# Optimization experiments

Measured on AMD Instinct MI355X. Metric: run time of the kernel, lower is better.

The kernel has to match this reference:

```python
import jax, jax.numpy as jnp
import numpy as np

DIM = 1024
HEADS = 16
DIM_HEAD = 64
INNER = HEADS * DIM_HEAD  # 1024
EPS = 1e-5


def layer_norm(x, gamma, beta):
    mu = jnp.mean(x, axis=-1, keepdims=True)
    var = jnp.mean(jnp.square(x - mu), axis=-1, keepdims=True)
    return (x - mu) * jax.lax.rsqrt(var + EPS) * gamma + beta


def setup_inputs() -> dict:
    key = jax.random.key(0)
    ks = jax.random.split(key, 6)
    b, n1, n2 = 8, 4096, 256
    x = jax.random.normal(ks[0], (b, n1, DIM), dtype=jnp.float32)
    latents = jax.random.normal(ks[1], (b, n2, DIM), dtype=jnp.float32)
    s = 1.0 / np.sqrt(DIM)
    Wq = jax.random.normal(ks[2], (DIM, INNER), dtype=jnp.float32) * s
    Wkv = jax.random.normal(ks[3], (DIM, 2 * INNER), dtype=jnp.float32) * s
    Wout = jax.random.normal(ks[4], (INNER, DIM), dtype=jnp.float32) * (1.0 / np.sqrt(INNER))
    g1 = jnp.ones((DIM,), jnp.float32); b1 = jnp.zeros((DIM,), jnp.float32)
    g2 = jnp.ones((DIM,), jnp.float32); b2 = jnp.zeros((DIM,), jnp.float32)
    return {"x": x, "latents": latents, "g1": g1, "b1": b1, "g2": g2, "b2": b2,
            "Wq": Wq, "Wkv": Wkv, "Wout": Wout}


def reference(x, latents, g1, b1, g2, b2, Wq, Wkv, Wout):
    b, l, _ = latents.shape
    xn = layer_norm(x, g1, b1)
    ln = layer_norm(latents, g2, b2)
    q = ln @ Wq  # (b, n2, inner)
    kv_input = jnp.concatenate([xn, ln], axis=1)  # (b, n1+n2, D)
    kv = kv_input @ Wkv
    k, v = jnp.split(kv, 2, axis=-1)
    # split heads -> (b, h, len, dh)
    def heads(t):
        return t.reshape(t.shape[0], t.shape[1], HEADS, DIM_HEAD).transpose(0, 2, 1, 3)
    q, k, v = heads(q), heads(k), heads(v)
    scale = 1.0 / np.sqrt(np.sqrt(DIM_HEAD))
    logits = jnp.einsum('bhqd,bhkd->bhqk', q * scale, k * scale)
    w = jax.nn.softmax(logits.astype(jnp.float32), axis=-1).astype(logits.dtype)
    out = jnp.einsum('bhqk,bhkd->bhqd', w, v)
    out = out.transpose(0, 2, 1, 3).reshape(b, l, INNER)
    return out @ Wout
```

## Files before the change

kernel.cpp:

```cpp
#include <hip/hip_runtime.h>
#include <hip/hip_bf16.h>

#define NB 8
#define N1 4096
#define N2 256
#define DIMD 1024
#define HEADS 16
#define DHD 64
#define KVLEN 4352
#define EPSF 1e-5f
#define L2E 1.44269504088896340736f

typedef __bf16 bf16x8 __attribute__((ext_vector_type(8)));
typedef float f32x4 __attribute__((ext_vector_type(4)));

__device__ __forceinline__ unsigned short f2bf(float f) {
  union { float f; unsigned int u; } v; v.f = f;
  return (unsigned short)((v.u + 0x7FFFu + ((v.u >> 16) & 1u)) >> 16);
}

__device__ __forceinline__ void gload_lds16(const void* g, void* l) {
  __builtin_amdgcn_global_load_lds(
      (const __attribute__((address_space(1))) void*)g,
      (__attribute__((address_space(3))) void*)l, 16, 0, 0);
}

__global__ __launch_bounds__(256) void ln_kernel(
    const float* __restrict__ in, const float* __restrict__ g, const float* __restrict__ bt,
    unsigned short* __restrict__ out, int rows_per_b, int out_off)
{
  int row = blockIdx.x;
  int b = row / rows_per_b;
  int r = row - b * rows_per_b;
  long orow = (long)b * KVLEN + out_off + r;
  const float* rp = in + (long)row * DIMD;
  int t = threadIdx.x;

  float4 x = *reinterpret_cast<const float4*>(rp + t * 4);
  float s = x.x + x.y + x.z + x.w;
  #pragma unroll
  for (int off = 1; off < 64; off <<= 1) s += __shfl_xor(s, off);
  __shared__ float red[8];
  int w = t >> 6;
  if ((t & 63) == 0) red[w] = s;
  __syncthreads();
  float mean = (red[0] + red[1] + red[2] + red[3]) * (1.0f / DIMD);

  float dx = x.x - mean, dy = x.y - mean, dz = x.z - mean, dw = x.w - mean;
  float sq = dx * dx + dy * dy + dz * dz + dw * dw;
  #pragma unroll
  for (int off = 1; off < 64; off <<= 1) sq += __shfl_xor(sq, off);
  if ((t & 63) == 0) red[4 + w] = sq;
  __syncthreads();
  float var = (red[4] + red[5] + red[6] + red[7]) * (1.0f / DIMD);
  float rs = rsqrtf(var + EPSF);

  float4 gg = *reinterpret_cast<const float4*>(g + t * 4);
  float4 bb = *reinterpret_cast<const float4*>(bt + t * 4);
  ushort4 o;
  o.x = f2bf(dx * rs * gg.x + bb.x);
  o.y = f2bf(dy * rs * gg.y + bb.y);
  o.z = f2bf(dz * rs * gg.z + bb.z);
  o.w = f2bf(dw * rs * gg.w + bb.w);
  *reinterpret_cast<ushort4*>(out + orow * DIMD + t * 4) = o;
}

__global__ __launch_bounds__(256) void transpose_bf16(
    const float* __restrict__ in, unsigned short* __restrict__ out, int R, int C)
{
  __shared__ float t[32][33];
  int r0 = blockIdx.y * 32, c0 = blockIdx.x * 32;
  int tx = threadIdx.x, ty = threadIdx.y;
  #pragma unroll
  for (int p = 0; p < 4; p++)
    t[ty + p * 8][tx] = in[(long)(r0 + ty + p * 8) * C + c0 + tx];
  __syncthreads();
  #pragma unroll
  for (int p = 0; p < 4; p++)
    out[(long)(c0 + ty + p * 8) * R + r0 + tx] = f2bf(t[tx][ty + p * 8]);
}

__global__ __launch_bounds__(256) void gemm2(
    const unsigned short* __restrict__ A, const unsigned short* __restrict__ BT,
    int M, int N, int K, int mode,
    unsigned short* __restrict__ obf, float* __restrict__ of32,
    unsigned short* __restrict__ kbuf, unsigned short* __restrict__ vbuf)
{
  __shared__ unsigned short As[128 * 32];
  __shared__ unsigned short Bs[128 * 32];
  int tid = threadIdx.x, l = tid & 63, w = tid >> 6;
  int m0 = blockIdx.y * 128, n0 = blockIdx.x * 128;
  int wm = w >> 1, wn = w & 1;
  int lrow = l & 15, lk = (l >> 4) * 8;

  int sr = l >> 2, scol = (l & 3) * 8;
  long am0 = m0 + w * 16 + sr, am1 = m0 + (w + 4) * 16 + sr;
  if (mode == 0) {
    am0 = (am0 >> 8) * KVLEN + N1 + (am0 & 255);
    am1 = (am1 >> 8) * KVLEN + N1 + (am1 & 255);
  }
  const unsigned short* gA0 = A + am0 * K + scol;
  const unsigned short* gA1 = A + am1 * K + scol;
  const unsigned short* gB0 = BT + (long)(n0 + w * 16 + sr) * K + scol;
  const unsigned short* gB1 = BT + (long)(n0 + (w + 4) * 16 + sr) * K + scol;
  unsigned short* lA0 = As + w * 512;
  unsigned short* lA1 = As + (w + 4) * 512;
  unsigned short* lB0 = Bs + w * 512;
  unsigned short* lB1 = Bs + (w + 4) * 512;

  f32x4 acc[4][4] = {};

  for (int k0 = 0; k0 < K; k0 += 32) {
    gload_lds16(gA0, lA0);
    gload_lds16(gA1, lA1);
    gload_lds16(gB0, lB0);
    gload_lds16(gB1, lB1);
    gA0 += 32; gA1 += 32; gB0 += 32; gB1 += 32;
    __syncthreads();
    bf16x8 af[4], bfr[4];
    #pragma unroll
    for (int i = 0; i < 4; i++)
      af[i] = *reinterpret_cast<bf16x8*>(&As[(wm * 64 + i * 16 + lrow) * 32 + lk]);
    #pragma unroll
    for (int j = 0; j < 4; j++)
      bfr[j] = *reinterpret_cast<bf16x8*>(&Bs[(wn * 64 + j * 16 + lrow) * 32 + lk]);
    #pragma unroll
    for (int i = 0; i < 4; i++)
      #pragma unroll
      for (int j = 0; j < 4; j++)
        acc[i][j] = __builtin_amdgcn_mfma_f32_16x16x32_bf16(af[i], bfr[j], acc[i][j], 0, 0, 0);
    __syncthreads();
  }

  #pragma unroll
  for (int i = 0; i < 4; i++)
    #pragma unroll
    for (int j = 0; j < 4; j++)
      #pragma unroll
      for (int r = 0; r < 4; r++) {
        int m = m0 + wm * 64 + i * 16 + (l >> 4) * 4 + r;
        int n = n0 + wn * 64 + j * 16 + (l & 15);
        float v = acc[i][j][r];
        if (mode == 0) {
          int b = m >> 8, qq = m & 255, h = n >> 6, d = n & 63;
          obf[(((long)(b * HEADS + h) * N2 + qq) << 6) + d] = f2bf(v);
        } else if (mode == 1) {
          int b = m / KVLEN, kk = m - b * KVLEN;
          unsigned short* dst; int nn;
          if (n < DIMD) { dst = kbuf; nn = n; } else { dst = vbuf; nn = n - DIMD; }
          int h = nn >> 6, d = nn & 63;
          dst[(((long)(b * HEADS + h) * KVLEN + kk) << 6) + d] = f2bf(v);
        } else {
          of32[(long)m * N + n] = v;
        }
      }
}

__global__ __launch_bounds__(256) void vtrans(
    const unsigned short* __restrict__ in, unsigned short* __restrict__ out)
{
  __shared__ unsigned short t[64][70];
  int bh = blockIdx.y, k0 = blockIdx.x * 64;
  int tid = threadIdx.x;
  const unsigned short* ip = in + ((long)bh * KVLEN + k0) * DHD;
  #pragma unroll
  for (int p = 0; p < 2; p++) {
    int eo = (tid + p * 256) * 8;
    int r = eo >> 6, c = eo & 63;
    *reinterpret_cast<bf16x8*>(&t[r][c]) =
        *reinterpret_cast<const bf16x8*>(ip + (long)r * DHD + c);
  }
  __syncthreads();
  unsigned short* op = out + (long)bh * DHD * KVLEN + k0;
  #pragma unroll
  for (int p = 0; p < 2; p++) {
    int eo = (tid + p * 256) * 8;
    int dd = eo >> 6, kc = eo & 63;
    ushort4 o0, o1;
    o0.x = t[kc + 0][dd]; o0.y = t[kc + 1][dd];
    o0.z = t[kc + 2][dd]; o0.w = t[kc + 3][dd];
    o1.x = t[kc + 4][dd]; o1.y = t[kc + 5][dd];
    o1.z = t[kc + 6][dd]; o1.w = t[kc + 7][dd];
    *reinterpret_cast<ushort4*>(op + (long)dd * KVLEN + kc) = o0;
    *reinterpret_cast<ushort4*>(op + (long)dd * KVLEN + kc + 4) = o1;
  }
}

__global__ __launch_bounds__(256) void attn_kernel(
    const unsigned short* __restrict__ qb, const unsigned short* __restrict__ kb,
    const unsigned short* __restrict__ vtb, unsigned short* __restrict__ attn)
{
  __shared__ unsigned short Ks[64][72];
  __shared__ unsigned short Vs[64][72];
  __shared__ unsigned short Ps[4][16][72];
  int qt = blockIdx.x, bh = blockIdx.y;
  int tid = threadIdx.x, l = tid & 63, w = tid >> 6;
  int lrow = l & 15, lk = (l >> 4) * 8;

  const unsigned short* qp = qb + ((long)bh * N2 + qt * 64 + w * 16) * DHD;
  const unsigned short* kp = kb + (long)bh * KVLEN * DHD;
  const unsigned short* vp = vtb + (long)bh * DHD * KVLEN;

  bf16x8 qa[2];
  qa[0] = *reinterpret_cast<const bf16x8*>(qp + lrow * DHD + lk);
  qa[1] = *reinterpret_cast<const bf16x8*>(qp + lrow * DHD + 32 + lk);

  f32x4 O[4] = {};
  float mrow[4] = {-1e30f, -1e30f, -1e30f, -1e30f};
  float lsum[4] = {0.f, 0.f, 0.f, 0.f};

  for (int blk = 0; blk < KVLEN / 64; blk++) {
    __syncthreads();
    #pragma unroll
    for (int p = 0; p < 2; p++) {
      int eo = (tid + p * 256) * 8;
      int row = eo >> 6, col = eo & 63;
      *reinterpret_cast<bf16x8*>(&Ks[row][col]) =
          *reinterpret_cast<const bf16x8*>(kp + (long)(blk * 64 + row) * DHD + col);
      *reinterpret_cast<bf16x8*>(&Vs[row][col]) =
          *reinterpret_cast<const bf16x8*>(vp + (long)row * KVLEN + blk * 64 + col);
    }
    __syncthreads();

    f32x4 S[4];
    #pragma unroll
    for (int nt = 0; nt < 4; nt++) {
      f32x4 s = {};
      #pragma unroll
      for (int kt = 0; kt < 2; kt++) {
        bf16x8 bk = *reinterpret_cast<bf16x8*>(&Ks[nt * 16 + lrow][kt * 32 + lk]);
        s = __builtin_amdgcn_mfma_f32_16x16x32_bf16(qa[kt], bk, s, 0, 0, 0);
      }
      S[nt] = s * 0.125f;
    }

    float mx[4], rsum[4];
    #pragma unroll
    for (int r = 0; r < 4; r++) {
      float v = fmaxf(fmaxf(S[0][r], S[1][r]), fmaxf(S[2][r], S[3][r]));
      #pragma unroll
      for (int off = 1; off < 16; off <<= 1) v = fmaxf(v, __shfl_xor(v, off));
      mx[r] = v;
    }
    float fac[4];
    #pragma unroll
    for (int r = 0; r < 4; r++) {
      float mn = fmaxf(mrow[r], mx[r]);
      fac[r] = exp2f((mrow[r] - mn) * L2E);
      mrow[r] = mn;
      rsum[r] = 0.f;
    }
    #pragma unroll
    for (int nt = 0; nt < 4; nt++)
      #pragma unroll
      for (int r = 0; r < 4; r++) {
        float p = exp2f((S[nt][r] - mrow[r]) * L2E);
        rsum[r] += p;
        Ps[w][(l >> 4) * 4 + r][nt * 16 + lrow] = f2bf(p);
      }
    #pragma unroll
    for (int r = 0; r < 4; r++) {
      float v = rsum[r];
      #pragma unroll
      for (int off = 1; off < 16; off <<= 1) v += __shfl_xor(v, off);
      lsum[r] = lsum[r] * fac[r] + v;
    }
    #pragma unroll
    for (int dt = 0; dt < 4; dt++)
      #pragma unroll
      for (int r = 0; r < 4; r++) O[dt][r] *= fac[r];

    asm volatile("s_waitcnt lgkmcnt(0)" ::: "memory");
    bf16x8 pa[2];
    pa[0] = *reinterpret_cast<bf16x8*>(&Ps[w][lrow][lk]);
    pa[1] = *reinterpret_cast<bf16x8*>(&Ps[w][lrow][32 + lk]);
    #pragma unroll
    for (int dt = 0; dt < 4; dt++)
      #pragma unroll
      for (int kt = 0; kt < 2; kt++) {
        bf16x8 bv = *reinterpret_cast<bf16x8*>(&Vs[dt * 16 + lrow][kt * 32 + lk]);
        O[dt] = __builtin_amdgcn_mfma_f32_16x16x32_bf16(pa[kt], bv, O[dt], 0, 0, 0);
      }
  }

  int b = bh >> 4, h = bh & 15;
  #pragma unroll
  for (int dt = 0; dt < 4; dt++)
    #pragma unroll
    for (int r = 0; r < 4; r++) {
      int grow = b * N2 + qt * 64 + w * 16 + (l >> 4) * 4 + r;
      int col = h * DHD + dt * 16 + lrow;
      attn[(long)grow * DIMD + col] = f2bf(O[dt][r] / lsum[r]);
    }
}

extern "C" void kernel_launch(void* const* d_in, const int* in_sizes, int n_in,
                              void* d_out, int out_size, void* d_ws, size_t ws_size,
                              hipStream_t stream) {
  const float* x    = (const float*)d_in[0];
  const float* lat  = (const float*)d_in[1];
  const float* g1   = (const float*)d_in[2];
  const float* b1   = (const float*)d_in[3];
  const float* g2   = (const float*)d_in[4];
  const float* b2   = (const float*)d_in[5];
  const float* Wq   = (const float*)d_in[6];
  const float* Wkv  = (const float*)d_in[7];
  const float* Wout = (const float*)d_in[8];
  float* out = (float*)d_out;

  char* ws = (char*)d_ws;
  size_t off = 0;
  auto alloc = [&](size_t bytes) -> void* {
    void* p = ws + off;
    off += (bytes + 255) & ~(size_t)255;
    return p;
  };
  unsigned short* kvin  = (unsigned short*)alloc((size_t)NB * KVLEN * DIMD * 2);
  unsigned short* WqT   = (unsigned short*)alloc((size_t)DIMD * DIMD * 2);
  unsigned short* WkvT  = (unsigned short*)alloc((size_t)2 * DIMD * DIMD * 2);
  unsigned short* WoutT = (unsigned short*)alloc((size_t)DIMD * DIMD * 2);
  unsigned short* qbuf  = (unsigned short*)alloc((size_t)NB * N2 * DIMD * 2);
  unsigned short* kbuf  = (unsigned short*)alloc((size_t)NB * HEADS * KVLEN * DHD * 2);
  unsigned short* vbuf  = (unsigned short*)alloc((size_t)NB * HEADS * KVLEN * DHD * 2);
  unsigned short* attn  = (unsigned short*)alloc((size_t)NB * N2 * DIMD * 2);
  if (off > ws_size) return;
  unsigned short* vtbuf = kvin;

  transpose_bf16<<<dim3(DIMD / 32, DIMD / 32), dim3(32, 8), 0, stream>>>(Wq, WqT, DIMD, DIMD);
  transpose_bf16<<<dim3(2 * DIMD / 32, DIMD / 32), dim3(32, 8), 0, stream>>>(Wkv, WkvT, DIMD, 2 * DIMD);
  transpose_bf16<<<dim3(DIMD / 32, DIMD / 32), dim3(32, 8), 0, stream>>>(Wout, WoutT, DIMD, DIMD);

  ln_kernel<<<NB * N1, 256, 0, stream>>>(x, g1, b1, kvin, N1, 0);
  ln_kernel<<<NB * N2, 256, 0, stream>>>(lat, g2, b2, kvin, N2, N1);

  gemm2<<<dim3(8, 16), 256, 0, stream>>>(kvin, WqT, NB * N2, DIMD, DIMD, 0,
                                         qbuf, nullptr, nullptr, nullptr);
  gemm2<<<dim3(16, 272), 256, 0, stream>>>(kvin, WkvT, NB * KVLEN, 2 * DIMD, DIMD, 1,
                                           nullptr, nullptr, kbuf, vbuf);
  vtrans<<<dim3(KVLEN / 64, NB * HEADS), 256, 0, stream>>>(vbuf, vtbuf);
  attn_kernel<<<dim3(4, NB * HEADS), 256, 0, stream>>>(qbuf, kbuf, vtbuf, attn);
  gemm2<<<dim3(8, 16), 256, 0, stream>>>(attn, WoutT, NB * N2, DIMD, DIMD, 2,
                                         nullptr, out, nullptr, nullptr);
}
```

Baseline: 709.3 us.

## Replace KV GEMM with pipelined 256x256 kernel fusing V transpose

The KV projection moves to a new 512-thread GEMM with 256x256 tiles, double-buffered LDS staged by direct global-to-LDS loads, XOR-swizzled LDS, and explicit barrier and priority scheduling. Its epilogue writes K in head layout and writes V already transposed through LDS, so the separate vtrans kernel and its round trip through memory go away. The Q and output GEMMs get narrower 128x64 tiles for more blocks, and the 1/8 softmax scale is folded into Q. The hand-written schedule raises register and LDS pressure to one block per CU, which could hurt latency hiding if the staging order is off.

```diff
diff --git a/kernel.cpp b/kernel.cpp
--- a/kernel.cpp
+++ b/kernel.cpp
@@ -80,17 +80,133 @@
     out[(long)(c0 + ty + p * 8) * R + r0 + tx] = f2bf(t[tx][ty + p * 8]);
 }
 
-__global__ __launch_bounds__(256) void gemm2(
+
+#define BARRIER8() { __builtin_amdgcn_sched_barrier(0); __builtin_amdgcn_s_barrier(); __builtin_amdgcn_sched_barrier(0); }
+#define VMW4() { asm volatile("s_waitcnt vmcnt(4)" ::: "memory"); __builtin_amdgcn_sched_barrier(0); }
+
+#define STG1(KIND, BUF, HALF, TILE, Q) \
+  gload_lds16((KIND ? BT : A) + \
+      (long)(((KIND) ? n0 : m0) + (HALF)*128 + w*16 + (Q)*8 + srow8) * 1024 + (TILE)*64 + sslot*8, \
+      lds + (KIND)*32768 + (BUF)*16384 + ((HALF)*128 + w*16 + (Q)*8)*64)
+#define STAGE8(KIND, BUF, HALF, TILE) { STG1(KIND,BUF,HALF,TILE,0); STG1(KIND,BUF,HALF,TILE,1); }
+
+#define LDA8(BUF) { _Pragma("unroll") for (int mt = 0; mt < 8; mt++) { \
+    int ar = wm*128 + mt*16 + lrow; \
+    af[mt][0] = *(const bf16x8*)&lds[(BUF)*16384 + ar*64 + ((l4) ^ (ar&7))*8]; \
+    af[mt][1] = *(const bf16x8*)&lds[(BUF)*16384 + ar*64 + ((4+l4) ^ (ar&7))*8]; } }
+
+#define LDB8(BUF, NT) { int br = wn*64 + (NT)*16 + lrow; \
+    bf0 = *(const bf16x8*)&lds[32768 + (BUF)*16384 + br*64 + ((l4) ^ (br&7))*8]; \
+    bf1 = *(const bf16x8*)&lds[32768 + (BUF)*16384 + br*64 + ((4+l4) ^ (br&7))*8]; }
+
+#define MM8(NT) { __builtin_amdgcn_s_setprio(1); \
+    _Pragma("unroll") for (int mt = 0; mt < 8; mt++) { \
+      acc[mt][NT] = __builtin_amdgcn_mfma_f32_16x16x32_bf16(af[mt][0], bf0, acc[mt][NT], 0, 0, 0); \
+      acc[mt][NT] = __builtin_amdgcn_mfma_f32_16x16x32_bf16(af[mt][1], bf1, acc[mt][NT], 0, 0, 0); } \
+    __builtin_amdgcn_s_setprio(0); }
+
+__global__ __launch_bounds__(512, 1) void gemm8(
     const unsigned short* __restrict__ A, const unsigned short* __restrict__ BT,
-    int M, int N, int K, int mode,
-    unsigned short* __restrict__ obf, float* __restrict__ of32,
-    unsigned short* __restrict__ kbuf, unsigned short* __restrict__ vbuf)
+    unsigned short* __restrict__ kbuf, unsigned short* __restrict__ vtbuf)
+{
+  __shared__ unsigned short lds[65536];
+  int tid = threadIdx.x, l = tid & 63, w = tid >> 6;
+  int wm = w >> 2, wn = w & 3;
+  int lrow = l & 15, l4 = l >> 4;
+  int bx = blockIdx.x, by = blockIdx.y;
+  int m0 = by * 256, n0 = bx * 256;
+  int srow8 = l >> 3;
+  int sslot = (l & 7) ^ srow8;
+
+  f32x4 acc[8][4] = {};
+  bf16x8 af[8][2];
+  bf16x8 bf0, bf1;
+
+  STAGE8(0, 0, 0, 0); STAGE8(0, 0, 1, 0);
+  STAGE8(1, 0, 0, 0); STAGE8(1, 0, 1, 0);
+  STAGE8(0, 1, 0, 1); STAGE8(0, 1, 1, 1);
+  VMW4(); BARRIER8();
+
+  for (int it = 0; it < 8; ++it) {
+    int t1 = 2 * it + 1;
+    int t2 = 2 * it + 2; if (t2 > 15) t2 = 15;
+    int t3 = 2 * it + 3; if (t3 > 15) t3 = 15;
+    LDA8(0); LDB8(0, 0);
+    STAGE8(1, 1, 0, t1);
+    BARRIER8(); MM8(0); BARRIER8();
+    LDB8(0, 1);
+    STAGE8(1, 1, 1, t1);
+    BARRIER8(); MM8(1); BARRIER8();
+    LDB8(0, 2);
+    STAGE8(0, 0, 0, t2);
+    BARRIER8(); MM8(2); BARRIER8();
+    LDB8(0, 3);
+    STAGE8(0, 0, 1, t2);
+    BARRIER8(); MM8(3); VMW4(); BARRIER8();
+    LDA8(1); LDB8(1, 0);
+    STAGE8(1, 0, 0, t2);
+    BARRIER8(); MM8(0); BARRIER8();
+    LDB8(1, 1);
+    STAGE8(1, 0, 1, t2);
+    BARRIER8(); MM8(1); BARRIER8();
+    LDB8(1, 2);
+    STAGE8(0, 1, 0, t3);
+    BARRIER8(); MM8(2); BARRIER8();
+    LDB8(1, 3);
+    STAGE8(0, 1, 1, t3);
+    BARRIER8(); MM8(3); VMW4(); BARRIER8();
+  }
+
+  __syncthreads();
+
+  int b = by / 17;
+  int kk0 = m0 - b * KVLEN;
+
+  if (n0 < DIMD) {
+    #pragma unroll
+    for (int mt = 0; mt < 8; mt++)
+      #pragma unroll
+      for (int nt = 0; nt < 4; nt++)
+        #pragma unroll
+        for (int r = 0; r < 4; r++) {
+          int kk = kk0 + wm * 128 + mt * 16 + l4 * 4 + r;
+          int h = bx * 4 + wn;
+          int d = nt * 16 + lrow;
+          kbuf[(((long)(b * HEADS + h) * KVLEN + kk) << 6) + d] = f2bf(acc[mt][nt][r]);
+        }
+  } else {
+    #pragma unroll
+    for (int mt = 0; mt < 8; mt++)
+      #pragma unroll
+      for (int nt = 0; nt < 4; nt++)
+        #pragma unroll
+        for (int r = 0; r < 4; r++) {
+          int nl = wn * 64 + nt * 16 + lrow;
+          int ml = wm * 128 + mt * 16 + l4 * 4 + r;
+          lds[nl * 256 + (ml ^ ((nl & 15) << 4))] = f2bf(acc[mt][nt][r]);
+        }
+    __syncthreads();
+    int nl = tid >> 1, mc = (tid & 1) * 128;
+    int h = bx * 4 + (nl >> 6) - HEADS;
+    int d = nl & 63;
+    unsigned short* op = vtbuf + ((long)(b * HEADS + h) * DHD + d) * KVLEN + kk0 + mc;
+    #pragma unroll
+    for (int j = 0; j < 16; j++) {
+      bf16x8 v = *(const bf16x8*)&lds[nl * 256 + ((mc + j * 8) ^ ((nl & 15) << 4))];
+      *(bf16x8*)(op + j * 8) = v;
+    }
+  }
+}
+
+__global__ __launch_bounds__(256) void gemm3(
+    const unsigned short* __restrict__ A, const unsigned short* __restrict__ BT,
+    int mode, unsigned short* __restrict__ obf, float* __restrict__ of32)
 {
   __shared__ unsigned short As[128 * 32];
-  __shared__ unsigned short Bs[128 * 32];
+  __shared__ unsigned short Bs[64 * 32];
+  const int K = DIMD;
   int tid = threadIdx.x, l = tid & 63, w = tid >> 6;
-  int m0 = blockIdx.y * 128, n0 = blockIdx.x * 128;
-  int wm = w >> 1, wn = w & 1;
+  int m0 = blockIdx.y * 128, n0 = blockIdx.x * 64;
   int lrow = l & 15, lk = (l >> 4) * 8;
 
   int sr = l >> 2, scol = (l & 3) * 8;
@@ -101,31 +217,28 @@
   }
   const unsigned short* gA0 = A + am0 * K + scol;
   const unsigned short* gA1 = A + am1 * K + scol;
-  const unsigned short* gB0 = BT + (long)(n0 + w * 16 + sr) * K + scol;
-  const unsigned short* gB1 = BT + (long)(n0 + (w + 4) * 16 + sr) * K + scol;
+  const unsigned short* gB = BT + (long)(n0 + w * 16 + sr) * K + scol;
   unsigned short* lA0 = As + w * 512;
   unsigned short* lA1 = As + (w + 4) * 512;
-  unsigned short* lB0 = Bs + w * 512;
-  unsigned short* lB1 = Bs + (w + 4) * 512;
-
-  f32x4 acc[4][4] = {};
+  unsigned short* lB = Bs + w * 512;
+
+  f32x4 acc[2][4] = {};
 
   for (int k0 = 0; k0 < K; k0 += 32) {
     gload_lds16(gA0, lA0);
     gload_lds16(gA1, lA1);
-    gload_lds16(gB0, lB0);
-    gload_lds16(gB1, lB1);
-    gA0 += 32; gA1 += 32; gB0 += 32; gB1 += 32;
+    gload_lds16(gB, lB);
+    gA0 += 32; gA1 += 32; gB += 32;
     __syncthreads();
-    bf16x8 af[4], bfr[4];
-    #pragma unroll
-    for (int i = 0; i < 4; i++)
-      af[i] = *reinterpret_cast<bf16x8*>(&As[(wm * 64 + i * 16 + lrow) * 32 + lk]);
+    bf16x8 af[2], bfr[4];
+    #pragma unroll
+    for (int i = 0; i < 2; i++)
+      af[i] = *reinterpret_cast<bf16x8*>(&As[(w * 32 + i * 16 + lrow) * 32 + lk]);
     #pragma unroll
     for (int j = 0; j < 4; j++)
-      bfr[j] = *reinterpret_cast<bf16x8*>(&Bs[(wn * 64 + j * 16 + lrow) * 32 + lk]);
-    #pragma unroll
-    for (int i = 0; i < 4; i++)
+      bfr[j] = *reinterpret_cast<bf16x8*>(&Bs[(j * 16 + lrow) * 32 + lk]);
+    #pragma unroll
+    for (int i = 0; i < 2; i++)
       #pragma unroll
       for (int j = 0; j < 4; j++)
         acc[i][j] = __builtin_amdgcn_mfma_f32_16x16x32_bf16(af[i], bfr[j], acc[i][j], 0, 0, 0);
@@ -133,57 +246,21 @@
   }
 
   #pragma unroll
-  for (int i = 0; i < 4; i++)
+  for (int i = 0; i < 2; i++)
     #pragma unroll
     for (int j = 0; j < 4; j++)
       #pragma unroll
       for (int r = 0; r < 4; r++) {
-        int m = m0 + wm * 64 + i * 16 + (l >> 4) * 4 + r;
-        int n = n0 + wn * 64 + j * 16 + (l & 15);
+        int m = m0 + w * 32 + i * 16 + (l >> 4) * 4 + r;
+        int n = n0 + j * 16 + lrow;
         float v = acc[i][j][r];
         if (mode == 0) {
           int b = m >> 8, qq = m & 255, h = n >> 6, d = n & 63;
-          obf[(((long)(b * HEADS + h) * N2 + qq) << 6) + d] = f2bf(v);
-        } else if (mode == 1) {
-          int b = m / KVLEN, kk = m - b * KVLEN;
-          unsigned short* dst; int nn;
-          if (n < DIMD) { dst = kbuf; nn = n; } else { dst = vbuf; nn = n - DIMD; }
-          int h = nn >> 6, d = nn & 63;
-          dst[(((long)(b * HEADS + h) * KVLEN + kk) << 6) + d] = f2bf(v);
+          obf[(((long)(b * HEADS + h) * N2 + qq) << 6) + d] = f2bf(v * 0.125f);
         } else {
-          of32[(long)m * N + n] = v;
+          of32[(long)m * DIMD + n] = v;
         }
       }
-}
-
-__global__ __launch_bounds__(256) void vtrans(
-    const unsigned short* __restrict__ in, unsigned short* __restrict__ out)
-{
-  __shared__ unsigned short t[64][70];
-  int bh = blockIdx.y, k0 = blockIdx.x * 64;
-  int tid = threadIdx.x;
-  const unsigned short* ip = in + ((long)bh * KVLEN + k0) * DHD;
-  #pragma unroll
-  for (int p = 0; p < 2; p++) {
-    int eo = (tid + p * 256) * 8;
-    int r = eo >> 6, c = eo & 63;
-    *reinterpret_cast<bf16x8*>(&t[r][c]) =
-        *reinterpret_cast<const bf16x8*>(ip + (long)r * DHD + c);
-  }
-  __syncthreads();
-  unsigned short* op = out + (long)bh * DHD * KVLEN + k0;
-  #pragma unroll
-  for (int p = 0; p < 2; p++) {
-    int eo = (tid + p * 256) * 8;
-    int dd = eo >> 6, kc = eo & 63;
-    ushort4 o0, o1;
-    o0.x = t[kc + 0][dd]; o0.y = t[kc + 1][dd];
-    o0.z = t[kc + 2][dd]; o0.w = t[kc + 3][dd];
-    o1.x = t[kc + 4][dd]; o1.y = t[kc + 5][dd];
-    o1.z = t[kc + 6][dd]; o1.w = t[kc + 7][dd];
-    *reinterpret_cast<ushort4*>(op + (long)dd * KVLEN + kc) = o0;
-    *reinterpret_cast<ushort4*>(op + (long)dd * KVLEN + kc + 4) = o1;
-  }
 }
 
 __global__ __launch_bounds__(256) void attn_kernel(
@@ -223,6 +300,7 @@
     __syncthreads();
 
     f32x4 S[4];
+    __builtin_amdgcn_s_setprio(1);
     #pragma unroll
     for (int nt = 0; nt < 4; nt++) {
       f32x4 s = {};
@@ -231,8 +309,9 @@
         bf16x8 bk = *reinterpret_cast<bf16x8*>(&Ks[nt * 16 + lrow][kt * 32 + lk]);
         s = __builtin_amdgcn_mfma_f32_16x16x32_bf16(qa[kt], bk, s, 0, 0, 0);
       }
-      S[nt] = s * 0.125f;
-    }
+      S[nt] = s;
+    }
+    __builtin_amdgcn_s_setprio(0);
 
     float mx[4], rsum[4];
     #pragma unroll
@@ -274,6 +353,7 @@
     bf16x8 pa[2];
     pa[0] = *reinterpret_cast<bf16x8*>(&Ps[w][lrow][lk]);
     pa[1] = *reinterpret_cast<bf16x8*>(&Ps[w][lrow][32 + lk]);
+    __builtin_amdgcn_s_setprio(1);
     #pragma unroll
     for (int dt = 0; dt < 4; dt++)
       #pragma unroll
@@ -281,6 +361,7 @@
         bf16x8 bv = *reinterpret_cast<bf16x8*>(&Vs[dt * 16 + lrow][kt * 32 + lk]);
         O[dt] = __builtin_amdgcn_mfma_f32_16x16x32_bf16(pa[kt], bv, O[dt], 0, 0, 0);
       }
+    __builtin_amdgcn_s_setprio(0);
   }
 
   int b = bh >> 4, h = bh & 15;
@@ -321,10 +402,9 @@
   unsigned short* WoutT = (unsigned short*)alloc((size_t)DIMD * DIMD * 2);
   unsigned short* qbuf  = (unsigned short*)alloc((size_t)NB * N2 * DIMD * 2);
   unsigned short* kbuf  = (unsigned short*)alloc((size_t)NB * HEADS * KVLEN * DHD * 2);
-  unsigned short* vbuf  = (unsigned short*)alloc((size_t)NB * HEADS * KVLEN * DHD * 2);
+  unsigned short* vtbuf = (unsigned short*)alloc((size_t)NB * HEADS * KVLEN * DHD * 2);
   unsigned short* attn  = (unsigned short*)alloc((size_t)NB * N2 * DIMD * 2);
   if (off > ws_size) return;
-  unsigned short* vtbuf = kvin;
 
   transpose_bf16<<<dim3(DIMD / 32, DIMD / 32), dim3(32, 8), 0, stream>>>(Wq, WqT, DIMD, DIMD);
   transpose_bf16<<<dim3(2 * DIMD / 32, DIMD / 32), dim3(32, 8), 0, stream>>>(Wkv, WkvT, DIMD, 2 * DIMD);
@@ -333,12 +413,8 @@
   ln_kernel<<<NB * N1, 256, 0, stream>>>(x, g1, b1, kvin, N1, 0);
   ln_kernel<<<NB * N2, 256, 0, stream>>>(lat, g2, b2, kvin, N2, N1);
 
-  gemm2<<<dim3(8, 16), 256, 0, stream>>>(kvin, WqT, NB * N2, DIMD, DIMD, 0,
-                                         qbuf, nullptr, nullptr, nullptr);
-  gemm2<<<dim3(16, 272), 256, 0, stream>>>(kvin, WkvT, NB * KVLEN, 2 * DIMD, DIMD, 1,
-                                           nullptr, nullptr, kbuf, vbuf);
-  vtrans<<<dim3(KVLEN / 64, NB * HEADS), 256, 0, stream>>>(vbuf, vtbuf);
+  gemm3<<<dim3(16, 16), 256, 0, stream>>>(kvin, WqT, 0, qbuf, nullptr);
+  gemm8<<<dim3(8, 136), 512, 0, stream>>>(kvin, WkvT, kbuf, vtbuf);
   attn_kernel<<<dim3(4, NB * HEADS), 256, 0, stream>>>(qbuf, kbuf, vtbuf, attn);
-  gemm2<<<dim3(8, 16), 256, 0, stream>>>(attn, WoutT, NB * N2, DIMD, DIMD, 2,
-                                         nullptr, out, nullptr, nullptr);
-}
+  gemm3<<<dim3(16, 16), 256, 0, stream>>>(attn, WoutT, 2, nullptr, out);
+}
```

After: 645.5 us. -9.0%, faster.
